# Kernel tuning notes

Hardware: AMD Instinct MI355X
Metric: run time of the kernel (lower is better)

## Reference

```python
import jax, jax.numpy as jnp
import numpy as np

# Static config matching init_kwargs
NUM_EXPERTS = 8
CAP_FACTOR = 1.0
MIN_CAP = 8


def setup_inputs() -> dict:
    key = jax.random.key(0)
    ks = jax.random.split(key, 10)
    G, S, D, H, E = 4, 4096, 1024, 4096, NUM_EXPERTS
    s = 0.02  # init stddev like nn.initializers.normal(0.02)
    return {
        "x": jax.random.normal(ks[0], (G, S, D), dtype=jnp.float32),
        "gate": jax.random.normal(ks[1], (D, E), dtype=jnp.float32) * s,
        "W1": jax.random.normal(ks[2], (E, D, H), dtype=jnp.float32) * s,
        "b1": jnp.zeros((E, H), dtype=jnp.float32),
        "W2": jax.random.normal(ks[3], (E, H, D), dtype=jnp.float32) * s,
        "b2": jnp.zeros((E, D), dtype=jnp.float32),
        "Ws1": jax.random.normal(ks[4], (D, H), dtype=jnp.float32) * s,
        "bs1": jnp.zeros((H,), dtype=jnp.float32),
        "Ws2": jax.random.normal(ks[5], (H, D), dtype=jnp.float32) * s,
        "bs2": jnp.zeros((D,), dtype=jnp.float32),
    }


def reference(x, gate, W1, b1, W2, b2, Ws1, bs1, Ws2, bs2):
    G, S, D = x.shape
    E = gate.shape[1]
    T = G * S
    capacity = max(MIN_CAP, int(CAP_FACTOR * T / E))  # static -> 2048

    # ---- Router (inference path: indices + scores, loss = 0) ----
    logits = jnp.einsum('gsd,de->gse', x, gate)           # (G,S,E)
    probs = jax.nn.softmax(logits, axis=-1)
    flat_probs = probs.transpose(2, 0, 1).reshape(E, T)    # (E,T)
    # capacity <= T here, so padding width is 0 (kept implicit)
    scores, token_idx = jax.lax.top_k(flat_probs, k=capacity)  # (E,C)
    scores = jnp.where(scores > -1e8, scores, 0.0)

    # ---- Routed experts: gather -> per-expert FFN (grouped GEMM) -> scatter-add
    flat_x = x.reshape(T, D)
    tok = flat_x[token_idx]                                # (E,C,D) gather
    h = jax.nn.gelu(jnp.einsum('ecd,edh->ech', tok, W1) + b1[:, None, :])
    out_tok = jnp.einsum('ech,ehd->ecd', h, W2) + b2[:, None, :]
    scaled = out_tok * scores[..., None]                   # weight by routing prob
    routed = jnp.zeros_like(flat_x).at[token_idx.reshape(-1)].add(
        scaled.reshape(E * capacity, D)).reshape(G, S, D)

    # ---- Shared expert (single FFN applied to all tokens) ----
    shared = jax.nn.gelu(jnp.einsum('gsd,dh->gsh', x, Ws1) + bs1)
    shared = jnp.einsum('gsh,hd->gsd', shared, Ws2) + bs2

    return routed + shared
```

## Files before the change

### kernel.cpp

```cpp
#include <hip/hip_runtime.h>
#include <hip/hip_bf16.h>

using bf16 = __hip_bfloat16;
typedef short v8s __attribute__((ext_vector_type(8)));
typedef float v4f __attribute__((ext_vector_type(4)));
typedef int v4i __attribute__((ext_vector_type(4)));

#define NE 8
#define NT 16384
#define ND 1024
#define NH 4096
#define CAP 2048

__device__ __forceinline__ void load_lds16(const void* g, void* s) {
  __builtin_amdgcn_global_load_lds(
      (const __attribute__((address_space(1))) unsigned int*)g,
      (__attribute__((address_space(3))) unsigned int*)s, 16, 0, 0);
}

__device__ __forceinline__ float gelu_tanh(float x) {
  float u = 0.7978845608028654f * (x + 0.044715f * x * x * x);
  float e = __expf(2.0f * u);
  float t = 1.0f - 2.0f / (e + 1.0f);
  return 0.5f * x * (1.0f + t);
}

__global__ __launch_bounds__(256) void tcvt(const float* __restrict__ src,
                                            bf16* __restrict__ dst, int R, int C) {
  __shared__ float tile[32][33];
  size_t mo = (size_t)blockIdx.z * R * C;
  int c0 = blockIdx.x * 32, r0 = blockIdx.y * 32;
  int tx = threadIdx.x & 31, ty = threadIdx.x >> 5;
  for (int i = ty; i < 32; i += 8)
    tile[i][tx] = src[mo + (size_t)(r0 + i) * C + c0 + tx];
  __syncthreads();
  for (int i = ty; i < 32; i += 8)
    dst[mo + (size_t)(c0 + i) * R + r0 + tx] = __float2bfloat16(tile[tx][i]);
}

template <typename T>
__global__ __launch_bounds__(256) void rowq(const T* __restrict__ in,
                                            signed char* __restrict__ q,
                                            float* __restrict__ sc,
                                            int L, int nrows) {
  int row = blockIdx.x * 4 + (threadIdx.x >> 6);
  if (row >= nrows) return;
  int lane = threadIdx.x & 63;
  const int epl = L >> 6;
  const T* src = in + (size_t)row * L + lane * epl;
  float m = 1e-30f;
  for (int i = 0; i < epl; i += 4) {
    float f0, f1, f2, f3;
    if constexpr (sizeof(T) == 2) {
      ushort4 u = *(const ushort4*)((const ushort*)src + i);
      f0 = __uint_as_float((unsigned)u.x << 16);
      f1 = __uint_as_float((unsigned)u.y << 16);
      f2 = __uint_as_float((unsigned)u.z << 16);
      f3 = __uint_as_float((unsigned)u.w << 16);
    } else {
      float4 v = *(const float4*)((const float*)src + i);
      f0 = v.x; f1 = v.y; f2 = v.z; f3 = v.w;
    }
    m = fmaxf(m, fmaxf(fmaxf(fabsf(f0), fabsf(f1)), fmaxf(fabsf(f2), fabsf(f3))));
  }
#pragma unroll
  for (int off = 32; off > 0; off >>= 1) m = fmaxf(m, __shfl_xor(m, off));
  float inv = 127.0f / m;
  signed char* dq = q + (size_t)row * L + lane * epl;
  for (int i = 0; i < epl; i += 4) {
    float f0, f1, f2, f3;
    if constexpr (sizeof(T) == 2) {
      ushort4 u = *(const ushort4*)((const ushort*)src + i);
      f0 = __uint_as_float((unsigned)u.x << 16);
      f1 = __uint_as_float((unsigned)u.y << 16);
      f2 = __uint_as_float((unsigned)u.z << 16);
      f3 = __uint_as_float((unsigned)u.w << 16);
    } else {
      float4 v = *(const float4*)((const float*)src + i);
      f0 = v.x; f1 = v.y; f2 = v.z; f3 = v.w;
    }
    int b0 = (int)rintf(f0 * inv), b1 = (int)rintf(f1 * inv);
    int b2 = (int)rintf(f2 * inv), b3 = (int)rintf(f3 * inv);
    unsigned pk = (unsigned)(b0 & 255) | ((unsigned)(b1 & 255) << 8) |
                  ((unsigned)(b2 & 255) << 16) | ((unsigned)(b3 & 255) << 24);
    *(unsigned*)(dq + i) = pk;
  }
  if (lane == 0) sc[row] = m * (1.0f / 127.0f);
}

__global__ __launch_bounds__(256) void router_k(const float* __restrict__ x,
                                                const float* __restrict__ gate,
                                                float* __restrict__ probs) {
  int wave = threadIdx.x >> 6, lane = threadIdx.x & 63;
  int t = blockIdx.x * 4 + wave;
  const float* xr = x + (size_t)t * ND;
  double acc[NE];
#pragma unroll
  for (int e = 0; e < NE; e++) acc[e] = 0.0;
  for (int d = lane; d < ND; d += 64) {
    double xv = (double)xr[d];
    const float* g = gate + d * NE;
#pragma unroll
    for (int e = 0; e < NE; e++) acc[e] += xv * (double)g[e];
  }
#pragma unroll
  for (int e = 0; e < NE; e++) {
    double v = acc[e];
#pragma unroll
    for (int off = 32; off > 0; off >>= 1) v += __shfl_xor(v, off);
    acc[e] = v;
  }
  if (lane == 0) {
    float l[NE], m = -1e30f;
#pragma unroll
    for (int e = 0; e < NE; e++) { l[e] = (float)acc[e]; m = fmaxf(m, l[e]); }
    float p[NE], s = 0.f;
#pragma unroll
    for (int e = 0; e < NE; e++) { p[e] = expf(l[e] - m); s += p[e]; }
#pragma unroll
    for (int e = 0; e < NE; e++) probs[e * NT + t] = p[e] / s;
  }
}

__global__ __launch_bounds__(1024) void topk_k(const float* __restrict__ probs,
                                               unsigned* __restrict__ thr_key,
                                               int* __restrict__ needed,
                                               int* __restrict__ cnt) {
  int e = blockIdx.x;
  const float* p = probs + e * NT;
  __shared__ int hist[256];
  __shared__ unsigned s_pref;
  __shared__ int s_rank;
  unsigned prefix = 0;
  int rank = CAP;
  for (int rd = 0; rd < 4; rd++) {
    int shift = 24 - rd * 8;
    if (threadIdx.x < 256) hist[threadIdx.x] = 0;
    __syncthreads();
    unsigned mask = (rd == 0) ? 0u : (0xFFFFFFFFu << (shift + 8));
    for (int t = threadIdx.x; t < NT; t += 1024) {
      unsigned k = __float_as_uint(p[t]);
      if ((k & mask) == prefix) atomicAdd(&hist[(k >> shift) & 255], 1);
    }
    __syncthreads();
    if (threadIdx.x == 0) {
      int cum = 0, b = 255;
      for (;;) {
        int c = hist[b];
        if (cum + c >= rank || b == 0) break;
        cum += c; b--;
      }
      s_pref = prefix | ((unsigned)b << shift);
      s_rank = rank - cum;
    }
    __syncthreads();
    prefix = s_pref; rank = s_rank;
    __syncthreads();
  }
  if (threadIdx.x == 0) {
    thr_key[e] = prefix; needed[e] = rank;
    cnt[e] = 0; cnt[NE + e] = 0;
  }
}

__global__ __launch_bounds__(256) void compact_k(const float* __restrict__ probs,
                                                 const unsigned* __restrict__ thr_key,
                                                 const int* __restrict__ needed,
                                                 int* __restrict__ cnt, int* __restrict__ eqc,
                                                 int* __restrict__ tok, float* __restrict__ scr) {
  int gid = blockIdx.x * 256 + threadIdx.x;
  int e = gid >> 14, t = gid & (NT - 1);
  float pv = probs[gid];
  unsigned k = __float_as_uint(pv);
  unsigned thr = thr_key[e];
  int nd = needed[e];
  bool gt = k > thr, eq = k == thr;
  unsigned long long mgt = __ballot(gt), meq = __ballot(eq);
  int lane = threadIdx.x & 63, wv = threadIdx.x >> 6;
  __shared__ int wcnt[2][4];
  __shared__ int base[2];
  if (lane == 0) { wcnt[0][wv] = __popcll(mgt); wcnt[1][wv] = __popcll(meq); }
  __syncthreads();
  if (threadIdx.x == 0) {
    int s0 = wcnt[0][0] + wcnt[0][1] + wcnt[0][2] + wcnt[0][3];
    int s1 = wcnt[1][0] + wcnt[1][1] + wcnt[1][2] + wcnt[1][3];
    base[0] = s0 ? atomicAdd(&cnt[e], s0) : 0;
    base[1] = s1 ? atomicAdd(&eqc[e], s1) : 0;
  }
  __syncthreads();
  unsigned long long lm = (1ull << lane) - 1ull;
  if (gt) {
    int p = __popcll(mgt & lm);
    for (int w = 0; w < wv; w++) p += wcnt[0][w];
    int slot = base[0] + p;
    tok[e * CAP + slot] = t; scr[e * CAP + slot] = pv;
  } else if (eq) {
    int q = base[1] + __popcll(meq & lm);
    for (int w = 0; w < wv; w++) q += wcnt[1][w];
    if (q < nd) {
      int slot = (CAP - nd) + q;
      tok[e * CAP + slot] = t; scr[e * CAP + slot] = pv;
    }
  }
}

#define BAR() __builtin_amdgcn_s_barrier()
#define SBAR0() __builtin_amdgcn_sched_barrier(0)

template <int MODE>
__global__ __launch_bounds__(512, 2) void gemm256(
    const bf16* __restrict__ A, int lda, const int* __restrict__ rowmap,
    const bf16* __restrict__ BT, long long bstride, int gshift,
    const float* __restrict__ bias, int bias_stride,
    int N, int K,
    bf16* __restrict__ outH, float* __restrict__ outF,
    const int* __restrict__ tok, const float* __restrict__ scr) {
  __shared__ __attribute__((aligned(16))) char lds[131072];
  const int tid = threadIdx.x;
  const int lane = tid & 63, wv = tid >> 6;
  const int wr = wv >> 2, wc = wv & 3;
  const int hw = blockIdx.y * gridDim.x + blockIdx.x;
  const int nwg = gridDim.x * gridDim.y;
  const int swz = (hw & 7) * (nwg >> 3) + (hw >> 3);
  const int m0 = (swz & 63) << 8;
  const int n0 = (swz >> 6) << 8;
  const int grp = m0 >> gshift;
  const bf16* Bp = BT + (size_t)grp * (size_t)bstride;
  const float* bp = bias + (size_t)grp * (size_t)bias_stride;
  const int nt = K >> 6;

  const int srow = tid >> 3;
  const int gc = (tid & 7) ^ (srow & 7);
  const bf16* srcA[4]; const bf16* srcB[4];
#pragma unroll
  for (int g = 0; g < 4; g++) {
    int am = m0 + g * 64 + srow;
    int ar = rowmap ? rowmap[am] : am;
    srcA[g] = A + (size_t)ar * lda + gc * 8;
    srcB[g] = Bp + (size_t)(n0 + g * 64 + srow) * K + gc * 8;
  }
  auto stageA = [&](int t, int h) {
    char* d = lds + ((t & 1) * 65536 + h * 16384) + tid * 16;
    load_lds16(srcA[h * 2 + 0] + (size_t)t * 64, d);
    load_lds16(srcA[h * 2 + 1] + (size_t)t * 64, d + 8192);
  };
  auto stageB = [&](int t, int h) {
    char* d = lds + ((t & 1) * 65536 + 32768 + h * 16384) + tid * 16;
    load_lds16(srcB[h * 2 + 0] + (size_t)t * 64, d);
    load_lds16(srcB[h * 2 + 1] + (size_t)t * 64, d + 8192);
  };

  const int fr = lane & 15, hi = lane >> 4;
  const int xr = fr & 7;
  const int cb0 = ((0 + hi) ^ xr) << 4;
  const int cb1 = ((4 + hi) ^ xr) << 4;
  const int arow = ((wr << 7) + fr) << 7;
  const int brow = ((wc << 6) + fr) << 7;

  v4f acc[8][4] = {};
  v8s a03[4][2], a47[4][2], b01[2][2], b23[2][2];

#define R_A03(BASE)                                                           \
  _Pragma("unroll") for (int mi = 0; mi < 4; mi++) {                          \
    a03[mi][0] = *(const v8s*)((BASE) + arow + mi * 2048 + cb0);              \
    a03[mi][1] = *(const v8s*)((BASE) + arow + mi * 2048 + cb1);              \
  }
#define R_A47(BASE)                                                           \
  _Pragma("unroll") for (int mi = 0; mi < 4; mi++) {                          \
    a47[mi][0] = *(const v8s*)((BASE) + arow + (4 + mi) * 2048 + cb0);        \
    a47[mi][1] = *(const v8s*)((BASE) + arow + (4 + mi) * 2048 + cb1);        \
  }
#define R_B01(BASE)                                                           \
  _Pragma("unroll") for (int ni = 0; ni < 2; ni++) {                          \
    b01[ni][0] = *(const v8s*)((BASE) + brow + ni * 2048 + cb0);              \
    b01[ni][1] = *(const v8s*)((BASE) + brow + ni * 2048 + cb1);              \
  }
#define R_B23(BASE)                                                           \
  _Pragma("unroll") for (int ni = 0; ni < 2; ni++) {                          \
    b23[ni][0] = *(const v8s*)((BASE) + brow + (2 + ni) * 2048 + cb0);        \
    b23[ni][1] = *(const v8s*)((BASE) + brow + (2 + ni) * 2048 + cb1);        \
  }
#define MFMA_Q(AB, BB, MOFF, NOFF)                                            \
  __builtin_amdgcn_s_setprio(1);                                              \
  _Pragma("unroll") for (int kk = 0; kk < 2; kk++)                            \
  _Pragma("unroll") for (int mi = 0; mi < 4; mi++)                            \
  _Pragma("unroll") for (int ni = 0; ni < 2; ni++)                            \
    acc[(MOFF) + mi][(NOFF) + ni] = __builtin_amdgcn_mfma_f32_16x16x32_bf16(  \
        AB[mi][kk], BB[ni][kk], acc[(MOFF) + mi][(NOFF) + ni], 0, 0, 0);      \
  __builtin_amdgcn_s_setprio(0);

  stageA(0, 0); stageA(0, 1); stageB(0, 0); stageB(0, 1);
  if (nt > 1) { stageB(1, 0); stageB(1, 1); }
  if (nt > 1) { asm volatile("s_waitcnt vmcnt(4)" ::: "memory"); }
  else        { asm volatile("s_waitcnt vmcnt(0)" ::: "memory"); }
  BAR();
  {
    const char* Ab0 = lds; const char* Bb0 = lds + 32768;
    R_A03(Ab0); R_B01(Bb0); R_B23(Bb0); R_A47(Ab0);
  }

  for (int t = 0; t < nt; ++t) {
    const char* AbN = lds + ((t + 1) & 1) * 65536;
    const char* BbN = AbN + 32768;
    asm volatile("s_waitcnt lgkmcnt(12)" ::: "memory"); SBAR0();
    MFMA_Q(a03, b01, 0, 0);
    if (t + 1 < nt) stageA(t + 1, 0);
    asm volatile("s_waitcnt lgkmcnt(8)" ::: "memory"); SBAR0();
    MFMA_Q(a03, b23, 0, 2);
    if (t + 1 < nt) stageA(t + 1, 1);
    BAR();
    asm volatile("s_waitcnt lgkmcnt(0)" ::: "memory"); SBAR0();
    MFMA_Q(a47, b01, 4, 0);
    if (t + 2 < nt) stageB(t + 2, 0);
    if (t + 2 < nt) stageB(t + 2, 1);
    if (t + 2 < nt) { asm volatile("s_waitcnt vmcnt(4)" ::: "memory"); }
    else            { asm volatile("s_waitcnt vmcnt(0)" ::: "memory"); }
    BAR();
    if (t + 1 < nt) { R_A03(AbN); R_B01(BbN); }
    MFMA_Q(a47, b23, 4, 2);
    if (t + 1 < nt) { R_B23(BbN); R_A47(AbN); }
  }
  asm volatile("s_waitcnt vmcnt(0) lgkmcnt(0)" ::: "memory");

  float bv[4];
#pragma unroll
  for (int ni = 0; ni < 4; ni++) bv[ni] = bp[n0 + (wc << 6) + ni * 16 + fr];
  const int rbase = m0 + (wr << 7) + (hi << 2);
#pragma unroll
  for (int mi = 0; mi < 8; mi++) {
#pragma unroll
    for (int r = 0; r < 4; r++) {
      int gm = rbase + mi * 16 + r;
      int trow = 0; float sv = 0.f;
      if (MODE == 2) { trow = tok[gm]; sv = scr[gm]; }
#pragma unroll
      for (int ni = 0; ni < 4; ni++) {
        int gn = n0 + (wc << 6) + ni * 16 + fr;
        float v = acc[mi][ni][r] + bv[ni];
        if (MODE == 0)      outH[(size_t)gm * N + gn] = __float2bfloat16(gelu_tanh(v));
        else if (MODE == 1) outF[(size_t)gm * N + gn] = v;
        else                atomicAdd(outF + (size_t)trow * N + gn, v * sv);
      }
    }
  }
}

__global__ __launch_bounds__(512, 2) void gemm256q(
    const signed char* __restrict__ A, int K, const int* __restrict__ rowmap,
    const signed char* __restrict__ BT, long long bstride, int gshift,
    const float* __restrict__ sxr, const float* __restrict__ swc, int sw_stride,
    const float* __restrict__ bias, int bias_stride, int N,
    bf16* __restrict__ outH) {
  __shared__ __attribute__((aligned(16))) char lds[131072];
  const int tid = threadIdx.x;
  const int lane = tid & 63, wv = tid >> 6;
  const int wr = wv >> 2, wc = wv & 3;
  const int m0 = blockIdx.y << 8, n0 = blockIdx.x << 8;
  const int grp = m0 >> gshift;
  const signed char* Bp = BT + (size_t)grp * (size_t)bstride;
  const float* bp = bias + (size_t)grp * (size_t)bias_stride;
  const float* swp = swc + (size_t)grp * (size_t)sw_stride;
  const int nt = K >> 7;

  const int srow = tid >> 3;
  const int gc = (tid & 7) ^ (srow & 7);
  const signed char* srcA[4]; const signed char* srcB[4];
#pragma unroll
  for (int g = 0; g < 4; g++) {
    int am = m0 + g * 64 + srow;
    int ar = rowmap ? rowmap[am] : am;
    srcA[g] = A + (size_t)ar * K + gc * 16;
    srcB[g] = Bp + (size_t)(n0 + g * 64 + srow) * K + gc * 16;
  }
  auto stageA = [&](int t, int h) {
    char* d = lds + ((t & 1) * 65536 + h * 16384) + tid * 16;
    load_lds16(srcA[h * 2 + 0] + (size_t)t * 128, d);
    load_lds16(srcA[h * 2 + 1] + (size_t)t * 128, d + 8192);
  };
  auto stageB = [&](int t, int h) {
    char* d = lds + ((t & 1) * 65536 + 32768 + h * 16384) + tid * 16;
    load_lds16(srcB[h * 2 + 0] + (size_t)t * 128, d);
    load_lds16(srcB[h * 2 + 1] + (size_t)t * 128, d + 8192);
  };

  const int fr = lane & 15, hi = lane >> 4;
  const int xr = fr & 7;
  const int cb0 = ((0 + hi) ^ xr) << 4;
  const int cb1 = ((4 + hi) ^ xr) << 4;
  const int arow = ((wr << 7) + fr) << 7;
  const int brow = ((wc << 6) + fr) << 7;

  v4i acc[8][4] = {};
  v4i a03[4][2], a47[4][2], b01[2][2], b23[2][2];

#define QR_A03(BASE)                                                          \
  _Pragma("unroll") for (int mi = 0; mi < 4; mi++) {                          \
    a03[mi][0] = *(const v4i*)((BASE) + arow + mi * 2048 + cb0);              \
    a03[mi][1] = *(const v4i*)((BASE) + arow + mi * 2048 + cb1);              \
  }
#define QR_A47(BASE)                                                          \
  _Pragma("unroll") for (int mi = 0; mi < 4; mi++) {                          \
    a47[mi][0] = *(const v4i*)((BASE) + arow + (4 + mi) * 2048 + cb0);        \
    a47[mi][1] = *(const v4i*)((BASE) + arow + (4 + mi) * 2048 + cb1);        \
  }
#define QR_B01(BASE)                                                          \
  _Pragma("unroll") for (int ni = 0; ni < 2; ni++) {                          \
    b01[ni][0] = *(const v4i*)((BASE) + brow + ni * 2048 + cb0);              \
    b01[ni][1] = *(const v4i*)((BASE) + brow + ni * 2048 + cb1);              \
  }
#define QR_B23(BASE)                                                          \
  _Pragma("unroll") for (int ni = 0; ni < 2; ni++) {                          \
    b23[ni][0] = *(const v4i*)((BASE) + brow + (2 + ni) * 2048 + cb0);        \
    b23[ni][1] = *(const v4i*)((BASE) + brow + (2 + ni) * 2048 + cb1);        \
  }
#define QMFMA_Q(AB, BB, MOFF, NOFF)                                           \
  __builtin_amdgcn_s_setprio(1);                                              \
  _Pragma("unroll") for (int kk = 0; kk < 2; kk++)                            \
  _Pragma("unroll") for (int mi = 0; mi < 4; mi++)                            \
  _Pragma("unroll") for (int ni = 0; ni < 2; ni++)                            \
    acc[(MOFF) + mi][(NOFF) + ni] = __builtin_amdgcn_mfma_i32_16x16x64_i8(    \
        AB[mi][kk], BB[ni][kk], acc[(MOFF) + mi][(NOFF) + ni], 0, 0, 0);      \
  __builtin_amdgcn_s_setprio(0);

  stageA(0, 0); stageA(0, 1); stageB(0, 0); stageB(0, 1);
  stageB(1, 0); stageB(1, 1);
  asm volatile("s_waitcnt vmcnt(4)" ::: "memory");
  BAR();
  {
    const char* Ab0 = lds; const char* Bb0 = lds + 32768;
    QR_A03(Ab0); QR_B01(Bb0); QR_B23(Bb0); QR_A47(Ab0);
  }

  for (int t = 0; t < nt; ++t) {
    const char* AbN = lds + ((t + 1) & 1) * 65536;
    const char* BbN = AbN + 32768;
    asm volatile("s_waitcnt lgkmcnt(12)" ::: "memory"); SBAR0();
    QMFMA_Q(a03, b01, 0, 0);
    if (t + 1 < nt) stageA(t + 1, 0);
    asm volatile("s_waitcnt lgkmcnt(8)" ::: "memory"); SBAR0();
    QMFMA_Q(a03, b23, 0, 2);
    if (t + 1 < nt) stageA(t + 1, 1);
    BAR();
    asm volatile("s_waitcnt lgkmcnt(0)" ::: "memory"); SBAR0();
    QMFMA_Q(a47, b01, 4, 0);
    if (t + 2 < nt) stageB(t + 2, 0);
    if (t + 2 < nt) stageB(t + 2, 1);
    if (t + 2 < nt) { asm volatile("s_waitcnt vmcnt(4)" ::: "memory"); }
    else            { asm volatile("s_waitcnt vmcnt(0)" ::: "memory"); }
    BAR();
    if (t + 1 < nt) { QR_A03(AbN); QR_B01(BbN); }
    QMFMA_Q(a47, b23, 4, 2);
    if (t + 1 < nt) { QR_B23(BbN); QR_A47(AbN); }
  }
  asm volatile("s_waitcnt vmcnt(0) lgkmcnt(0)" ::: "memory");

  float bv[4], swv[4];
#pragma unroll
  for (int ni = 0; ni < 4; ni++) {
    int gn = n0 + (wc << 6) + ni * 16 + fr;
    bv[ni] = bp[gn]; swv[ni] = swp[gn];
  }
  const int rbase = m0 + (wr << 7) + (hi << 2);
#pragma unroll
  for (int mi = 0; mi < 8; mi++) {
#pragma unroll
    for (int r = 0; r < 4; r++) {
      int gm = rbase + mi * 16 + r;
      float sxa = sxr[rowmap ? rowmap[gm] : gm];
#pragma unroll
      for (int ni = 0; ni < 4; ni++) {
        int gn = n0 + (wc << 6) + ni * 16 + fr;
        float v = (float)acc[mi][ni][r] * (sxa * swv[ni]) + bv[ni];
        outH[(size_t)gm * N + gn] = __float2bfloat16(gelu_tanh(v));
      }
    }
  }
}

extern "C" void kernel_launch(void* const* d_in, const int* in_sizes, int n_in,
                              void* d_out, int out_size, void* d_ws, size_t ws_size,
                              hipStream_t stream) {
  const float* x   = (const float*)d_in[0];
  const float* gate= (const float*)d_in[1];
  const float* W1  = (const float*)d_in[2];
  const float* b1  = (const float*)d_in[3];
  const float* W2  = (const float*)d_in[4];
  const float* b2  = (const float*)d_in[5];
  const float* Ws1 = (const float*)d_in[6];
  const float* bs1 = (const float*)d_in[7];
  const float* Ws2 = (const float*)d_in[8];
  const float* bs2 = (const float*)d_in[9];
  float* out = (float*)d_out;

  char* w = (char*)d_ws;
  size_t off = 0;
  auto alloc = [&](size_t bytes) {
    void* p = w + off;
    off = (off + bytes + 255) & ~(size_t)255;
    return p;
  };
  bf16* w1T   = (bf16*)alloc((size_t)NE * NH * ND * 2);
  bf16* w2T   = (bf16*)alloc((size_t)NE * ND * NH * 2);
  bf16* ws1T  = (bf16*)alloc((size_t)NH * ND * 2);
  bf16* ws2T  = (bf16*)alloc((size_t)ND * NH * 2);
  bf16* h     = (bf16*)alloc((size_t)NT * NH * 2);
  signed char* xq   = (signed char*)alloc((size_t)NT * ND);
  signed char* w1q  = (signed char*)alloc((size_t)NE * NH * ND);
  signed char* ws1q = (signed char*)alloc((size_t)NH * ND);
  float* sx   = (float*)alloc((size_t)NT * 4);
  float* sw1  = (float*)alloc((size_t)NE * NH * 4);
  float* sws1 = (float*)alloc((size_t)NH * 4);
  float* probs= (float*)alloc((size_t)NE * NT * 4);
  unsigned* thr = (unsigned*)alloc(NE * 4);
  int* needed = (int*)alloc(NE * 4);
  int* cnt    = (int*)alloc(2 * NE * 4);
  int* eqc    = cnt + NE;
  int* tok    = (int*)alloc((size_t)NE * CAP * 4);
  float* scr  = (float*)alloc((size_t)NE * CAP * 4);
  (void)alloc(65536);
  if (off > ws_size) return;

  tcvt<<<dim3(NH / 32, ND / 32, NE), 256, 0, stream>>>(W1, w1T, ND, NH);
  tcvt<<<dim3(ND / 32, NH / 32, NE), 256, 0, stream>>>(W2, w2T, NH, ND);
  tcvt<<<dim3(NH / 32, ND / 32, 1), 256, 0, stream>>>(Ws1, ws1T, ND, NH);
  tcvt<<<dim3(ND / 32, NH / 32, 1), 256, 0, stream>>>(Ws2, ws2T, NH, ND);

  rowq<float><<<NT / 4, 256, 0, stream>>>(x, xq, sx, ND, NT);
  rowq<ushort><<<NE * NH / 4, 256, 0, stream>>>((const ushort*)w1T, w1q, sw1, ND, NE * NH);
  rowq<ushort><<<NH / 4, 256, 0, stream>>>((const ushort*)ws1T, ws1q, sws1, ND, NH);

  router_k<<<NT / 4, 256, 0, stream>>>(x, gate, probs);
  topk_k<<<NE, 1024, 0, stream>>>(probs, thr, needed, cnt);
  compact_k<<<NE * NT / 256, 256, 0, stream>>>(probs, thr, needed, cnt, eqc, tok, scr);

  gemm256q<<<dim3(NH / 256, NT / 256), 512, 0, stream>>>(
      xq, ND, nullptr, ws1q, 0, 30, sx, sws1, 0, bs1, 0, NH, h);
  gemm256<1><<<dim3(ND / 256, NT / 256), 512, 0, stream>>>(
      h, NH, nullptr, ws2T, 0, 30, bs2, 0, ND, NH, nullptr, out, nullptr, nullptr);

  gemm256q<<<dim3(NH / 256, NT / 256), 512, 0, stream>>>(
      xq, ND, tok, w1q, (long long)NH * ND, 11, sx, sw1, NH, b1, NH, NH, h);
  gemm256<2><<<dim3(ND / 256, NT / 256), 512, 0, stream>>>(
      h, NH, nullptr, w2T, (long long)ND * NH, 11, b2, ND, ND, NH, nullptr, out, tok, scr);
}
```

Before: 839.5 us.

## Quantize W1 directly from fp32 with fused transpose and add XCD-aware tile swizzle

Drops the intermediate bf16 transpose of W1/Ws1 followed by a row-quantize pass. A column-max kernel now computes the per-output scales straight from fp32, and a transpose-quantize kernel writes int8 directly, cutting roughly a full read/write of the expert weight matrices. The bf16 transpose for W2/Ws2 uses larger 128x64 tiles with packed stores. Both GEMMs switch to a swizzle that gives each XCD a contiguous block of M tiles, aiming at better L2 reuse. The column-max kernel reads with a stride of a full row, which may be poorly coalesced, and quantization now starts from fp32 values instead of bf16-rounded ones, so results can differ slightly.

```diff
diff --git a/kernel.cpp b/kernel.cpp
--- a/kernel.cpp
+++ b/kernel.cpp
@@ -25,62 +25,76 @@
   return 0.5f * x * (1.0f + t);
 }
 
-__global__ __launch_bounds__(256) void tcvt(const float* __restrict__ src,
-                                            bf16* __restrict__ dst, int R, int C) {
-  __shared__ float tile[32][33];
+__global__ __launch_bounds__(256) void tcvt64(const float* __restrict__ src,
+                                              bf16* __restrict__ dst, int R, int C) {
+  __shared__ float tile[128][65];
   size_t mo = (size_t)blockIdx.z * R * C;
-  int c0 = blockIdx.x * 32, r0 = blockIdx.y * 32;
-  int tx = threadIdx.x & 31, ty = threadIdx.x >> 5;
-  for (int i = ty; i < 32; i += 8)
-    tile[i][tx] = src[mo + (size_t)(r0 + i) * C + c0 + tx];
+  int c0 = blockIdx.x * 64, r0 = blockIdx.y * 128;
+  int lane = threadIdx.x & 63, wv = threadIdx.x >> 6;
+  for (int i = wv; i < 128; i += 4)
+    tile[i][lane] = src[mo + (size_t)(r0 + i) * C + c0 + lane];
   __syncthreads();
-  for (int i = ty; i < 32; i += 8)
-    dst[mo + (size_t)(c0 + i) * R + r0 + tx] = __float2bfloat16(tile[tx][i]);
-}
-
-template <typename T>
-__global__ __launch_bounds__(256) void rowq(const T* __restrict__ in,
-                                            signed char* __restrict__ q,
-                                            float* __restrict__ sc,
-                                            int L, int nrows) {
+  for (int j = wv; j < 64; j += 4) {
+    bf16 o0 = __float2bfloat16(tile[2 * lane][j]);
+    bf16 o1 = __float2bfloat16(tile[2 * lane + 1][j]);
+    ushort2 pk = make_ushort2(*(unsigned short*)&o0, *(unsigned short*)&o1);
+    *(ushort2*)((unsigned short*)dst + mo + (size_t)(c0 + j) * R + r0 + 2 * lane) = pk;
+  }
+}
+
+__global__ __launch_bounds__(256) void colmax_k(const float* __restrict__ src,
+                                                float* __restrict__ sc, int R, int C) {
+  size_t mo = (size_t)blockIdx.y * R * C;
+  int c = blockIdx.x * 256 + threadIdx.x;
+  const float* p = src + mo + c;
+  float m = 1e-30f;
+#pragma unroll 8
+  for (int r = 0; r < R; r++) m = fmaxf(m, fabsf(p[(size_t)r * C]));
+  sc[(size_t)blockIdx.y * C + c] = m * (1.0f / 127.0f);
+}
+
+__global__ __launch_bounds__(256) void tq_k(const float* __restrict__ src,
+                                            const float* __restrict__ scl,
+                                            signed char* __restrict__ dst, int R, int C) {
+  __shared__ float tile[128][65];
+  size_t mo = (size_t)blockIdx.z * R * C;
+  size_t so = (size_t)blockIdx.z * C;
+  int c0 = blockIdx.x * 64, r0 = blockIdx.y * 128;
+  int lane = threadIdx.x & 63, wv = threadIdx.x >> 6;
+  for (int i = wv; i < 128; i += 4)
+    tile[i][lane] = src[mo + (size_t)(r0 + i) * C + c0 + lane];
+  __syncthreads();
+  for (int j = wv; j < 64; j += 4) {
+    float inv = 1.0f / scl[so + c0 + j];
+    int b0 = (int)rintf(tile[2 * lane][j] * inv);
+    int b1 = (int)rintf(tile[2 * lane + 1][j] * inv);
+    unsigned short pk = (unsigned short)((b0 & 255) | ((b1 & 255) << 8));
+    *(unsigned short*)(dst + mo + (size_t)(c0 + j) * R + r0 + 2 * lane) = pk;
+  }
+}
+
+__global__ __launch_bounds__(256) void rowq_f(const float* __restrict__ in,
+                                              signed char* __restrict__ q,
+                                              float* __restrict__ sc,
+                                              int L, int nrows) {
   int row = blockIdx.x * 4 + (threadIdx.x >> 6);
   if (row >= nrows) return;
   int lane = threadIdx.x & 63;
   const int epl = L >> 6;
-  const T* src = in + (size_t)row * L + lane * epl;
+  const float* src = in + (size_t)row * L + lane * epl;
   float m = 1e-30f;
   for (int i = 0; i < epl; i += 4) {
-    float f0, f1, f2, f3;
-    if constexpr (sizeof(T) == 2) {
-      ushort4 u = *(const ushort4*)((const ushort*)src + i);
-      f0 = __uint_as_float((unsigned)u.x << 16);
-      f1 = __uint_as_float((unsigned)u.y << 16);
-      f2 = __uint_as_float((unsigned)u.z << 16);
-      f3 = __uint_as_float((unsigned)u.w << 16);
-    } else {
-      float4 v = *(const float4*)((const float*)src + i);
-      f0 = v.x; f1 = v.y; f2 = v.z; f3 = v.w;
-    }
-    m = fmaxf(m, fmaxf(fmaxf(fabsf(f0), fabsf(f1)), fmaxf(fabsf(f2), fabsf(f3))));
+    float4 v = *(const float4*)(src + i);
+    m = fmaxf(m, fmaxf(fmaxf(fabsf(v.x), fabsf(v.y)), fmaxf(fabsf(v.z), fabsf(v.w))));
   }
 #pragma unroll
   for (int off = 32; off > 0; off >>= 1) m = fmaxf(m, __shfl_xor(m, off));
   float inv = 127.0f / m;
   signed char* dq = q + (size_t)row * L + lane * epl;
   for (int i = 0; i < epl; i += 4) {
-    float f0, f1, f2, f3;
-    if constexpr (sizeof(T) == 2) {
-      ushort4 u = *(const ushort4*)((const ushort*)src + i);
-      f0 = __uint_as_float((unsigned)u.x << 16);
-      f1 = __uint_as_float((unsigned)u.y << 16);
-      f2 = __uint_as_float((unsigned)u.z << 16);
-      f3 = __uint_as_float((unsigned)u.w << 16);
-    } else {
-      float4 v = *(const float4*)((const float*)src + i);
-      f0 = v.x; f1 = v.y; f2 = v.z; f3 = v.w;
-    }
-    int b0 = (int)rintf(f0 * inv), b1 = (int)rintf(f1 * inv);
-    int b2 = (int)rintf(f2 * inv), b3 = (int)rintf(f3 * inv);
+    float4 v = *(const float4*)(src + i);
+    int b0 = (int)rintf(v.x * inv), b1 = (int)rintf(v.y * inv);
+    int b2 = (int)rintf(v.z * inv), b3 = (int)rintf(v.w * inv);
     unsigned pk = (unsigned)(b0 & 255) | ((unsigned)(b1 & 255) << 8) |
                   ((unsigned)(b2 & 255) << 16) | ((unsigned)(b3 & 255) << 24);
     *(unsigned*)(dq + i) = pk;
@@ -207,6 +221,17 @@
 #define BAR() __builtin_amdgcn_s_barrier()
 #define SBAR0() __builtin_amdgcn_sched_barrier(0)
 
+#define XCD_SWZ(m0, n0)                                                       \
+  const int hw_ = blockIdx.y * gridDim.x + blockIdx.x;                        \
+  const int ntx_ = gridDim.x;                                                 \
+  const int chunk_ = gridDim.y >> 3;                                          \
+  const int xcd_ = hw_ & 7;                                                   \
+  const int i2_ = hw_ >> 3;                                                   \
+  const int lm_ = i2_ / ntx_;                                                 \
+  const int ln_ = i2_ - lm_ * ntx_;                                           \
+  const int m0 = (xcd_ * chunk_ + lm_) << 8;                                  \
+  const int n0 = ln_ << 8;
+
 template <int MODE>
 __global__ __launch_bounds__(512, 2) void gemm256(
     const bf16* __restrict__ A, int lda, const int* __restrict__ rowmap,
@@ -219,11 +244,7 @@
   const int tid = threadIdx.x;
   const int lane = tid & 63, wv = tid >> 6;
   const int wr = wv >> 2, wc = wv & 3;
-  const int hw = blockIdx.y * gridDim.x + blockIdx.x;
-  const int nwg = gridDim.x * gridDim.y;
-  const int swz = (hw & 7) * (nwg >> 3) + (hw >> 3);
-  const int m0 = (swz & 63) << 8;
-  const int n0 = (swz >> 6) << 8;
+  XCD_SWZ(m0, n0);
   const int grp = m0 >> gshift;
   const bf16* Bp = BT + (size_t)grp * (size_t)bstride;
   const float* bp = bias + (size_t)grp * (size_t)bias_stride;
@@ -355,7 +376,7 @@
   const int tid = threadIdx.x;
   const int lane = tid & 63, wv = tid >> 6;
   const int wr = wv >> 2, wc = wv & 3;
-  const int m0 = blockIdx.y << 8, n0 = blockIdx.x << 8;
+  XCD_SWZ(m0, n0);
   const int grp = m0 >> gshift;
   const signed char* Bp = BT + (size_t)grp * (size_t)bstride;
   const float* bp = bias + (size_t)grp * (size_t)bias_stride;
@@ -499,9 +520,7 @@
     off = (off + bytes + 255) & ~(size_t)255;
     return p;
   };
-  bf16* w1T   = (bf16*)alloc((size_t)NE * NH * ND * 2);
   bf16* w2T   = (bf16*)alloc((size_t)NE * ND * NH * 2);
-  bf16* ws1T  = (bf16*)alloc((size_t)NH * ND * 2);
   bf16* ws2T  = (bf16*)alloc((size_t)ND * NH * 2);
   bf16* h     = (bf16*)alloc((size_t)NT * NH * 2);
   signed char* xq   = (signed char*)alloc((size_t)NT * ND);
@@ -520,14 +539,13 @@
   (void)alloc(65536);
   if (off > ws_size) return;
 
-  tcvt<<<dim3(NH / 32, ND / 32, NE), 256, 0, stream>>>(W1, w1T, ND, NH);
-  tcvt<<<dim3(ND / 32, NH / 32, NE), 256, 0, stream>>>(W2, w2T, NH, ND);
-  tcvt<<<dim3(NH / 32, ND / 32, 1), 256, 0, stream>>>(Ws1, ws1T, ND, NH);
-  tcvt<<<dim3(ND / 32, NH / 32, 1), 256, 0, stream>>>(Ws2, ws2T, NH, ND);
-
-  rowq<float><<<NT / 4, 256, 0, stream>>>(x, xq, sx, ND, NT);
-  rowq<ushort><<<NE * NH / 4, 256, 0, stream>>>((const ushort*)w1T, w1q, sw1, ND, NE * NH);
-  rowq<ushort><<<NH / 4, 256, 0, stream>>>((const ushort*)ws1T, ws1q, sws1, ND, NH);
+  tcvt64<<<dim3(ND / 64, NH / 128, NE), 256, 0, stream>>>(W2, w2T, NH, ND);
+  tcvt64<<<dim3(ND / 64, NH / 128, 1), 256, 0, stream>>>(Ws2, ws2T, NH, ND);
+  colmax_k<<<dim3(NH / 256, NE), 256, 0, stream>>>(W1, sw1, ND, NH);
+  colmax_k<<<dim3(NH / 256, 1), 256, 0, stream>>>(Ws1, sws1, ND, NH);
+  tq_k<<<dim3(NH / 64, ND / 128, NE), 256, 0, stream>>>(W1, sw1, w1q, ND, NH);
+  tq_k<<<dim3(NH / 64, ND / 128, 1), 256, 0, stream>>>(Ws1, sws1, ws1q, ND, NH);
+  rowq_f<<<NT / 4, 256, 0, stream>>>(x, xq, sx, ND, NT);
 
   router_k<<<NT / 4, 256, 0, stream>>>(x, gate, probs);
   topk_k<<<NE, 1024, 0, stream>>>(probs, thr, needed, cnt);
```

New measurement: 899.6 us. +7.2%, slower.
